# Kernel optimization log

Hardware: AMD Instinct MI355X
Metric: run time of the kernel (lower is better)

## Reference

```python
import jax, jax.numpy as jnp
import numpy as np

N = 768
W = 224
H = 126
FX = 2343.0242837919386 * W / 2560.0   # 205.01462483179463
FY = 2343.0242837919386 * H / 1440.0   # same value


def quat_to_rot(quats):
    """[N,4] wxyz quaternions -> [N,3,3] rotation matrices."""
    q = quats / jnp.linalg.norm(quats, axis=1, keepdims=True)
    w, x, y, z = q[:, 0], q[:, 1], q[:, 2], q[:, 3]
    R = jnp.stack([
        jnp.stack([1 - 2 * (y * y + z * z), 2 * (x * y - z * w), 2 * (x * z + y * w)], axis=-1),
        jnp.stack([2 * (x * y + z * w), 1 - 2 * (x * x + z * z), 2 * (y * z - x * w)], axis=-1),
        jnp.stack([2 * (x * z - y * w), 2 * (y * z + x * w), 1 - 2 * (x * x + y * y)], axis=-1),
    ], axis=1)
    return R


def setup_inputs() -> dict:
    key = jax.random.key(0)
    k1, k2, k3, k4, k5 = jax.random.split(key, 5)
    # gaussians in front of the camera (z in [4,8])
    means_xy = jax.random.uniform(k1, (N, 2), minval=-2.0, maxval=2.0)
    means_z = jax.random.uniform(k2, (N, 1), minval=4.0, maxval=8.0)
    means = jnp.concatenate([means_xy, means_z], axis=1).astype(jnp.float32)
    scales_raw = jnp.log(jax.random.uniform(k3, (N, 3), minval=0.01, maxval=0.05)).astype(jnp.float32)
    quats = jax.random.normal(k4, (N, 4), dtype=jnp.float32)
    opac_raw = jax.random.normal(k5, (N,), dtype=jnp.float32)

    # precomputed buffers (torch.no_grad in original)
    Rg = quat_to_rot(quats)                      # [N,3,3]
    M = Rg * jnp.exp(scales_raw)[:, None, :]     # R @ diag(exp(scales))
    cov_world = M @ jnp.swapaxes(M, 1, 2)        # [N,3,3]
    means_hom = jnp.concatenate([means, jnp.ones((N, 1), jnp.float32)], axis=1)  # [N,4]
    means_hom_tmp = means_hom.T[None]            # [1,4,N]
    opacities_rast = jax.nn.sigmoid(opac_raw)[None, None, :, None]  # [1,1,N,1]
    K = jnp.array([[FX, 0.0, W / 2.0], [0.0, FY, H / 2.0], [0.0, 0.0, 1.0]], jnp.float32)
    X, Y = jnp.meshgrid(jnp.arange(W), jnp.arange(H), indexing='xy')  # [H,W]
    tile_coord = jnp.stack([X, Y], axis=-1).reshape(-1, 2).astype(jnp.float32)[None, :, None, :]  # [1,HW,1,2]
    lim_x = jnp.array([1.3 * 0.5 * W / FX], jnp.float32)
    lim_y = jnp.array([1.3 * 0.5 * H / FY], jnp.float32)

    # camera pose: small rotation about z + small translation, bottom row [0,0,0,1]
    ang = 0.05
    c, s = np.cos(ang), np.sin(ang)
    pose = np.eye(4, dtype=np.float32)
    pose[:3, :3] = np.array([[c, -s, 0.0], [s, c, 0.0], [0.0, 0.0, 1.0]], np.float32)
    pose[:3, 3] = np.array([0.1, -0.1, 0.3], np.float32)
    x = jnp.asarray(pose)[None]                  # [1,4,4]

    return {"x": x, "means_hom_tmp": means_hom_tmp, "cov_world": cov_world,
            "opacities_rast": opacities_rast, "K": K, "tile_coord": tile_coord,
            "lim_x": lim_x, "lim_y": lim_y, "fx": float(FX), "fy": float(FY)}


def reference(x, means_hom_tmp, cov_world, opacities_rast, K, tile_coord, lim_x, lim_y, fx, fy):
    mh = means_hom_tmp[0]                                  # [4,N]
    means_cam_hom = jnp.einsum('bij,jn->bni', x, mh)       # [B,N,4]
    means_cam = means_cam_hom[:, :, :3] / means_cam_hom[:, :, 3:4]
    R_cam = x[:, :3, :3]                                   # [B,3,3]
    cov_cam = jnp.einsum('bij,njk,blk->bnil', R_cam, cov_world, R_cam)  # [B,N,3,3]
    means_proj_hom = jnp.einsum('bni,ji->bnj', means_cam, K)
    means2D = means_proj_hom[:, :, :2] / means_proj_hom[:, :, 2:3]      # [B,N,2]

    xc, yc, z = means_cam[:, :, 0], means_cam[:, :, 1], means_cam[:, :, 2]
    tx = z * jnp.minimum(lim_x, jnp.maximum(-lim_x, xc / z))
    ty = z * jnp.minimum(lim_y, jnp.maximum(-lim_y, yc / z))
    J00 = fx / z
    J02 = -fx * tx / z ** 2
    J11 = fy / z
    J12 = -fy * ty / z ** 2
    cc = cov_cam
    c00 = J00 * J00 * cc[:, :, 0, 0] + J00 * J02 * cc[:, :, 0, 2] + J02 * J00 * cc[:, :, 2, 0] + J02 * J02 * cc[:, :, 2, 2] + 0.3
    c11 = J11 * J11 * cc[:, :, 1, 1] + J11 * J12 * cc[:, :, 1, 2] + J12 * J11 * cc[:, :, 2, 1] + J12 * J12 * cc[:, :, 2, 2] + 0.3
    c01 = J00 * J11 * cc[:, :, 0, 1] + J00 * J12 * cc[:, :, 0, 2] + J02 * J11 * cc[:, :, 2, 1] + J02 * J12 * cc[:, :, 2, 2]
    c10 = J11 * J00 * cc[:, :, 1, 0] + J11 * J02 * cc[:, :, 1, 2] + J12 * J00 * cc[:, :, 2, 0] + J12 * J02 * cc[:, :, 2, 2]
    inv_det = 1.0 / (c00 * c11 - c01 * c10)
    conic00 = inv_det * c11
    conic01 = -inv_det * c01
    conic10 = -inv_det * c10
    conic11 = inv_det * c00

    # brute-force per-pixel rasterization: [B,HW,N,2]
    dx = tile_coord - means2D[:, None, :, :]
    power = -0.5 * (dx[..., 0] ** 2 * conic00[:, None, :]
                    + dx[..., 1] ** 2 * conic11[:, None, :]
                    + dx[..., 0] * dx[..., 1] * (conic01 + conic10)[:, None, :])
    gauss_weight = jnp.exp(power)                          # [B,HW,N]
    alpha = gauss_weight[..., None] * opacities_rast       # [B,HW,N,1]
    alpha_clip = 0.99 - jax.nn.relu(0.99 - alpha)          # == -relu(-alpha+0.99)+0.99
    return alpha_clip
```

## Files before the change

### kernel.cpp

```cpp
#include <hip/hip_runtime.h>
#include <hip/hip_bf16.h>

#define NGAUSS 768
#define IMW 224
#define IMH 126
#define NPIX (IMW * IMH)
#define GPT 4
#define VPP (NGAUSS / GPT)
#define NBLOCKS 1536
#define NTHREADS 256
#define TOTTHREADS (NBLOCKS * NTHREADS)
#define PSTRIDE (TOTTHREADS / VPP)

typedef float vfloat4 __attribute__((ext_vector_type(4)));

__device__ __forceinline__ float ldf(const void* p, int idx, bool bf) {
  if (bf) {
    unsigned int u = (unsigned int)((const unsigned short*)p)[idx];
    union { unsigned int u; float f; } c; c.u = u << 16;
    return c.f;
  }
  return ((const float*)p)[idx];
}

__global__ __launch_bounds__(NTHREADS) void raster_kernel(
    const void* __restrict__ x_in,
    const void* __restrict__ mh_in,
    const void* __restrict__ cov_in,
    const void* __restrict__ op_in,
    const void* __restrict__ K_in,
    const void* __restrict__ limx_in,
    const void* __restrict__ limy_in,
    const void* __restrict__ fx_in,
    const void* __restrict__ fy_in,
    float* __restrict__ out)
{
  __shared__ float sP[6][NGAUSS];

  const unsigned int* mhu = (const unsigned int*)mh_in;
  bool bf = (mhu[1152] == 0x3F803F80u) && (mhu[1153] == 0x3F803F80u);

  float K00 = ldf(K_in, 0, bf), K01 = ldf(K_in, 1, bf), K02 = ldf(K_in, 2, bf);
  float K10 = ldf(K_in, 3, bf), K11 = ldf(K_in, 4, bf), K12 = ldf(K_in, 5, bf);
  float K20 = ldf(K_in, 6, bf), K21 = ldf(K_in, 7, bf), K22 = ldf(K_in, 8, bf);

  float fxv, fyv;
  {
    unsigned int u = *(const unsigned int*)fx_in;
    union { unsigned int u; float f; } a, b; a.u = u; b.u = u << 16;
    fxv = (a.f > 190.0f && a.f < 220.0f) ? a.f
        : ((b.f > 190.0f && b.f < 220.0f) ? b.f : K00);
  }
  {
    unsigned int u = *(const unsigned int*)fy_in;
    union { unsigned int u; float f; } a, b; a.u = u; b.u = u << 16;
    fyv = (a.f > 190.0f && a.f < 220.0f) ? a.f
        : ((b.f > 190.0f && b.f < 220.0f) ? b.f : K11);
  }
  float limx = ldf(limx_in, 0, bf);
  float limy = ldf(limy_in, 0, bf);

  float X[4][4];
#pragma unroll
  for (int i = 0; i < 4; ++i)
#pragma unroll
    for (int j = 0; j < 4; ++j) X[i][j] = ldf(x_in, 4 * i + j, bf);

  const float S = -0.5f * 1.44269504088896340736f;

  for (int n = threadIdx.x; n < NGAUSS; n += NTHREADS) {
    float m0 = ldf(mh_in, 0 * NGAUSS + n, bf);
    float m1 = ldf(mh_in, 1 * NGAUSS + n, bf);
    float m2 = ldf(mh_in, 2 * NGAUSS + n, bf);
    float m3 = ldf(mh_in, 3 * NGAUSS + n, bf);

    float h0 = X[0][0]*m0 + X[0][1]*m1 + X[0][2]*m2 + X[0][3]*m3;
    float h1 = X[1][0]*m0 + X[1][1]*m1 + X[1][2]*m2 + X[1][3]*m3;
    float h2 = X[2][0]*m0 + X[2][1]*m1 + X[2][2]*m2 + X[2][3]*m3;
    float h3 = X[3][0]*m0 + X[3][1]*m1 + X[3][2]*m2 + X[3][3]*m3;
    float iw = 1.0f / h3;
    float mcx = h0 * iw, mcy = h1 * iw, mcz = h2 * iw;

    float cw[3][3];
#pragma unroll
    for (int i = 0; i < 3; ++i)
#pragma unroll
      for (int j = 0; j < 3; ++j) cw[i][j] = ldf(cov_in, n * 9 + 3 * i + j, bf);

    float T[3][3];
#pragma unroll
    for (int i = 0; i < 3; ++i)
#pragma unroll
      for (int j = 0; j < 3; ++j)
        T[i][j] = X[i][0]*cw[0][j] + X[i][1]*cw[1][j] + X[i][2]*cw[2][j];
    float cc[3][3];
#pragma unroll
    for (int i = 0; i < 3; ++i)
#pragma unroll
      for (int l = 0; l < 3; ++l)
        cc[i][l] = T[i][0]*X[l][0] + T[i][1]*X[l][1] + T[i][2]*X[l][2];

    float ph0 = K00*mcx + K01*mcy + K02*mcz;
    float ph1 = K10*mcx + K11*mcy + K12*mcz;
    float ph2 = K20*mcx + K21*mcy + K22*mcz;
    float ipz = 1.0f / ph2;
    float m2x = ph0 * ipz, m2y = ph1 * ipz;

    float z = mcz;
    float invz = 1.0f / z;
    float tx = z * fminf(limx, fmaxf(-limx, mcx * invz));
    float ty = z * fminf(limy, fmaxf(-limy, mcy * invz));
    float J00 = fxv * invz;
    float J02 = -fxv * tx * invz * invz;
    float J11 = fyv * invz;
    float J12 = -fyv * ty * invz * invz;

    float c00 = J00*J00*cc[0][0] + J00*J02*cc[0][2] + J02*J00*cc[2][0] + J02*J02*cc[2][2] + 0.3f;
    float c11 = J11*J11*cc[1][1] + J11*J12*cc[1][2] + J12*J11*cc[2][1] + J12*J12*cc[2][2] + 0.3f;
    float c01 = J00*J11*cc[0][1] + J00*J12*cc[0][2] + J02*J11*cc[2][1] + J02*J12*cc[2][2];
    float c10 = J11*J00*cc[1][0] + J11*J02*cc[1][2] + J12*J00*cc[2][0] + J12*J02*cc[2][2];

    float invdet = 1.0f / (c00 * c11 - c01 * c10);
    float con00 = invdet * c11;
    float con01 = -invdet * c01;
    float con10 = -invdet * c10;
    float con11 = invdet * c00;

    sP[0][n] = m2x;
    sP[1][n] = m2y;
    sP[2][n] = S * con00;
    sP[3][n] = S * (con01 + con10);
    sP[4][n] = S * con11;
    sP[5][n] = ldf(op_in, n, bf);
  }
  __syncthreads();

  int tid = blockIdx.x * NTHREADS + threadIdx.x;
  int v = tid % VPP;
  int p = tid / VPP;
  int n0 = v * GPT;

  float mx[GPT], my[GPT], A[GPT], B[GPT], C[GPT], O[GPT];
#pragma unroll
  for (int i = 0; i < GPT; ++i) {
    mx[i] = sP[0][n0 + i];
    my[i] = sP[1][n0 + i];
    A[i]  = sP[2][n0 + i];
    B[i]  = sP[3][n0 + i];
    C[i]  = sP[4][n0 + i];
    O[i]  = sP[5][n0 + i];
  }

  int px = p % IMW, py = p / IMW;
  const int dpx = PSTRIDE % IMW;
  const int dpy = PSTRIDE / IMW;
  for (; p < NPIX; p += PSTRIDE) {
    float fpx = (float)px, fpy = (float)py;
    float r[GPT];
#pragma unroll
    for (int i = 0; i < GPT; ++i) {
      float dx = fpx - mx[i];
      float dy = fpy - my[i];
      float pw = fmaf(dx, fmaf(A[i], dx, B[i] * dy), C[i] * dy * dy);
      r[i] = fminf(__builtin_amdgcn_exp2f(pw) * O[i], 0.99f);
    }
    vfloat4 val = { r[0], r[1], r[2], r[3] };
    *(vfloat4*)(out + (size_t)p * NGAUSS + n0) = val;

    px += dpx; py += dpy;
    if (px >= IMW) { px -= IMW; py += 1; }
  }
}

extern "C" void kernel_launch(void* const* d_in, const int* in_sizes, int n_in,
                              void* d_out, int out_size, void* d_ws, size_t ws_size,
                              hipStream_t stream) {
  (void)in_sizes; (void)n_in; (void)d_ws; (void)ws_size; (void)out_size;
  raster_kernel<<<NBLOCKS, NTHREADS, 0, stream>>>(
      d_in[0], d_in[1], d_in[2], d_in[3], d_in[4],
      d_in[6], d_in[7], d_in[8], d_in[9],
      (float*)d_out);
}
```

Measured before the change: 115.9 us.

## Split gaussians into per-block groups to avoid redundant preprocessing

```diff
diff --git a/kernel.cpp b/kernel.cpp
--- a/kernel.cpp
+++ b/kernel.cpp
@@ -6,11 +6,14 @@
 #define IMH 126
 #define NPIX (IMW * IMH)
 #define GPT 4
-#define VPP (NGAUSS / GPT)
-#define NBLOCKS 1536
+#define GPB 64
+#define NGRP (NGAUSS / GPB)
+#define CPB (GPB / GPT)
 #define NTHREADS 256
-#define TOTTHREADS (NBLOCKS * NTHREADS)
-#define PSTRIDE (TOTTHREADS / VPP)
+#define PROWS (NTHREADS / CPB)
+#define NPBLK 128
+#define NBLOCKS (NGRP * NPBLK)
+#define PSTRIDE (NPBLK * PROWS)
 
 typedef float vfloat4 __attribute__((ext_vector_type(4)));
 
@@ -35,40 +38,45 @@
     const void* __restrict__ fy_in,
     float* __restrict__ out)
 {
-  __shared__ float sP[6][NGAUSS];
+  __shared__ float sP[6][GPB];
 
-  const unsigned int* mhu = (const unsigned int*)mh_in;
-  bool bf = (mhu[1152] == 0x3F803F80u) && (mhu[1153] == 0x3F803F80u);
+  const int g    = blockIdx.x % NGRP;
+  const int pblk = blockIdx.x / NGRP;
 
-  float K00 = ldf(K_in, 0, bf), K01 = ldf(K_in, 1, bf), K02 = ldf(K_in, 2, bf);
-  float K10 = ldf(K_in, 3, bf), K11 = ldf(K_in, 4, bf), K12 = ldf(K_in, 5, bf);
-  float K20 = ldf(K_in, 6, bf), K21 = ldf(K_in, 7, bf), K22 = ldf(K_in, 8, bf);
+  if (threadIdx.x < GPB) {
+    const int n = g * GPB + threadIdx.x;
 
-  float fxv, fyv;
-  {
-    unsigned int u = *(const unsigned int*)fx_in;
-    union { unsigned int u; float f; } a, b; a.u = u; b.u = u << 16;
-    fxv = (a.f > 190.0f && a.f < 220.0f) ? a.f
-        : ((b.f > 190.0f && b.f < 220.0f) ? b.f : K00);
-  }
-  {
-    unsigned int u = *(const unsigned int*)fy_in;
-    union { unsigned int u; float f; } a, b; a.u = u; b.u = u << 16;
-    fyv = (a.f > 190.0f && a.f < 220.0f) ? a.f
-        : ((b.f > 190.0f && b.f < 220.0f) ? b.f : K11);
-  }
-  float limx = ldf(limx_in, 0, bf);
-  float limy = ldf(limy_in, 0, bf);
+    const unsigned int* mhu = (const unsigned int*)mh_in;
+    bool bf = (mhu[1152] == 0x3F803F80u) && (mhu[1153] == 0x3F803F80u);
 
-  float X[4][4];
+    float K00 = ldf(K_in, 0, bf), K01 = ldf(K_in, 1, bf), K02 = ldf(K_in, 2, bf);
+    float K10 = ldf(K_in, 3, bf), K11 = ldf(K_in, 4, bf), K12 = ldf(K_in, 5, bf);
+    float K20 = ldf(K_in, 6, bf), K21 = ldf(K_in, 7, bf), K22 = ldf(K_in, 8, bf);
+
+    float fxv, fyv;
+    {
+      unsigned int u = *(const unsigned int*)fx_in;
+      union { unsigned int u; float f; } a, b; a.u = u; b.u = u << 16;
+      fxv = (a.f > 190.0f && a.f < 220.0f) ? a.f
+          : ((b.f > 190.0f && b.f < 220.0f) ? b.f : K00);
+    }
+    {
+      unsigned int u = *(const unsigned int*)fy_in;
+      union { unsigned int u; float f; } a, b; a.u = u; b.u = u << 16;
+      fyv = (a.f > 190.0f && a.f < 220.0f) ? a.f
+          : ((b.f > 190.0f && b.f < 220.0f) ? b.f : K11);
+    }
+    float limx = ldf(limx_in, 0, bf);
+    float limy = ldf(limy_in, 0, bf);
+
+    float X[4][4];
 #pragma unroll
-  for (int i = 0; i < 4; ++i)
+    for (int i = 0; i < 4; ++i)
 #pragma unroll
-    for (int j = 0; j < 4; ++j) X[i][j] = ldf(x_in, 4 * i + j, bf);
+      for (int j = 0; j < 4; ++j) X[i][j] = ldf(x_in, 4 * i + j, bf);
 
-  const float S = -0.5f * 1.44269504088896340736f;
+    const float S = -0.5f * 1.44269504088896340736f;
 
-  for (int n = threadIdx.x; n < NGAUSS; n += NTHREADS) {
     float m0 = ldf(mh_in, 0 * NGAUSS + n, bf);
     float m1 = ldf(mh_in, 1 * NGAUSS + n, bf);
     float m2 = ldf(mh_in, 2 * NGAUSS + n, bf);
@@ -126,31 +134,33 @@
     float con10 = -invdet * c10;
     float con11 = invdet * c00;
 
-    sP[0][n] = m2x;
-    sP[1][n] = m2y;
-    sP[2][n] = S * con00;
-    sP[3][n] = S * (con01 + con10);
-    sP[4][n] = S * con11;
-    sP[5][n] = ldf(op_in, n, bf);
+    int t = threadIdx.x;
+    sP[0][t] = m2x;
+    sP[1][t] = m2y;
+    sP[2][t] = S * con00;
+    sP[3][t] = S * (con01 + con10);
+    sP[4][t] = S * con11;
+    sP[5][t] = ldf(op_in, n, bf);
   }
   __syncthreads();
 
-  int tid = blockIdx.x * NTHREADS + threadIdx.x;
-  int v = tid % VPP;
-  int p = tid / VPP;
-  int n0 = v * GPT;
+  const int chunk = threadIdx.x & (CPB - 1);
+  const int prow  = threadIdx.x >> 4;
+  const int nl0   = chunk * GPT;
+  const int n0    = g * GPB + nl0;
 
   float mx[GPT], my[GPT], A[GPT], B[GPT], C[GPT], O[GPT];
 #pragma unroll
   for (int i = 0; i < GPT; ++i) {
-    mx[i] = sP[0][n0 + i];
-    my[i] = sP[1][n0 + i];
-    A[i]  = sP[2][n0 + i];
-    B[i]  = sP[3][n0 + i];
-    C[i]  = sP[4][n0 + i];
-    O[i]  = sP[5][n0 + i];
+    mx[i] = sP[0][nl0 + i];
+    my[i] = sP[1][nl0 + i];
+    A[i]  = sP[2][nl0 + i];
+    B[i]  = sP[3][nl0 + i];
+    C[i]  = sP[4][nl0 + i];
+    O[i]  = sP[5][nl0 + i];
   }
 
+  int p = pblk * PROWS + prow;
   int px = p % IMW, py = p / IMW;
   const int dpx = PSTRIDE % IMW;
   const int dpy = PSTRIDE / IMW;
```

Result: faster. 111.5 us (-3.8%).
